# Performance work log

Measured on AMD Instinct MI355X. Metric: run time of the kernel, lower is better.

The kernel has to match this reference:

```python
import jax, jax.numpy as jnp
import numpy as np

B, L, LA, LL = 256, 512, 8, 64
V, D, P, HOPS = 100000, 300, 3, 3


def setup_inputs() -> dict:
    key = jax.random.key(0)
    ks = jax.random.split(key, 18)
    sc = 0.05
    return {
        "text":   jax.random.randint(ks[0], (B, L),  0, V),
        "aspect": jax.random.randint(ks[1], (B, LA), 0, V),
        "left":   jax.random.randint(ks[2], (B, LL), 0, V),
        # pretrained embedding table
        "embed": jax.random.normal(ks[3], (V, D), jnp.float32) * 0.1,
        # all Linear weights stored as [in, out] (y = x @ W + b)
        "Wx": jax.random.normal(ks[4], (D, D), jnp.float32) * sc,   # x_linear (no bias)
        "Ws": jax.random.normal(ks[5], (D, D), jnp.float32) * sc,   # s_linear (no bias)
        "Wk": jax.random.normal(ks[6], (D, D), jnp.float32) * sc,   # attention w_k
        "bk": jnp.zeros((D,), jnp.float32),
        "Wq": jax.random.normal(ks[7], (D, D), jnp.float32) * sc,   # attention w_q
        "bq": jnp.zeros((D,), jnp.float32),
        "w_mlp": jax.random.normal(ks[8], (2 * D,), jnp.float32) * sc,  # attention mlp score vector
        "Wproj": jax.random.normal(ks[9], (D, D), jnp.float32) * sc,    # attention proj
        "bproj": jnp.zeros((D,), jnp.float32),
        "Wm": jax.random.normal(ks[10], (D, D), jnp.float32) * sc,  # mlp
        "bm": jnp.zeros((D,), jnp.float32),
        "Wd": jax.random.normal(ks[11], (D, P), jnp.float32) * sc,  # dense
        "bd": jnp.zeros((P,), jnp.float32),
    }


def _forward(text, aspect, left, embed, Wx, Ws, Wk, bk, Wq, bq, w_mlp,
             Wproj, bproj, Wm, bm, Wd, bd):
    f32 = jnp.float32
    left_len = (left != 0).sum(-1)    # (B,)
    mem_len = (text != 0).sum(-1)     # (B,)
    asp_len = (aspect != 0).sum(-1)   # (B,)
    mem_len_f = mem_len.astype(f32)

    # aspect mean-pooled query (sum over all positions / nonzero count, as in torch code)
    asp_e = embed[aspect].sum(1) / asp_len.astype(f32)[:, None]   # (B, D)
    x = asp_e[:, None, :]                                         # (B, 1, D)

    memory = embed[text]                                          # (B, L, D)
    v_s = (memory.sum(1) / mem_len_f[:, None])[:, None, :]        # (B, 1, D)

    # SqueezeEmbedding (zero padding) + vectorized locationed_memory decay
    idx = jnp.arange(L, dtype=f32)[None, :]                       # (1, L)
    start = (left_len - asp_len).astype(f32)[:, None]             # aspect_start
    end = left_len.astype(f32)[:, None]                           # aspect_end
    l = jnp.where(idx < start, start - idx,
                  jnp.where(idx <= end, 0.0, idx - end))          # (B, L)
    w = 1.0 - l / mem_len_f[:, None]
    w = jnp.where(idx < mem_len_f[:, None], w, 0.0)               # zero padded positions
    memory = memory * w[:, :, None]                               # (B, L, D)

    for _ in range(HOPS):
        x = x @ Wx                                                # (B, 1, D)
        s = v_s @ Ws                                              # computed but unused (faithful)
        # Attention(score_function='mlp', n_head=1, hidden=D)
        kx = memory @ Wk + bk                                     # (B, L, D)
        qx = x @ Wq + bq                                          # (B, 1, D)
        # tanh(cat(kx, qx) @ w_mlp) == tanh(kx@w1 + qx@w2)
        score = jnp.tanh(kx @ w_mlp[:D] + qx @ w_mlp[D:])         # (B, L)
        score = jax.nn.softmax(score, axis=-1)
        v_ts = jnp.einsum('bl,bld->bd', score, kx)[:, None, :]    # (B, 1, D)
        v_ts = v_ts @ Wproj + bproj

    v_ns = (v_ts + v_s).reshape(text.shape[0], -1)                # (B, D)
    v_ms = jnp.tanh(v_ns @ Wm + bm)
    out = jax.nn.softmax(v_ms @ Wd + bd, axis=-1)                 # (B, P)
    return out


def reference(text, aspect, left, embed, Wx, Ws, Wk, bk, Wq, bq, w_mlp,
              Wproj, bproj, Wm, bm, Wd, bd):
    return _forward(text, aspect, left, embed, Wx, Ws, Wk, bk, Wq, bq,
                    w_mlp, Wproj, bproj, Wm, bm, Wd, bd)
```

## Files before the change

### kernel.cpp

```cpp
#include <hip/hip_runtime.h>
#include <math.h>

#define WS_KV 0
#define WS_C0 300
#define WS_C1 301
#define WS_H0 304
#define WS_H1 604
#define WS_MW 1024
#define WS_VS 77824

__device__ __forceinline__ float wred(float v) {
#pragma unroll
    for (int off = 32; off > 0; off >>= 1) v += __shfl_xor(v, off);
    return v;
}

__global__ __launch_bounds__(64) void k_prep(
    const float* __restrict__ Wk, const float* __restrict__ bk,
    const float* __restrict__ Wq, const float* __restrict__ bq,
    const float* __restrict__ wmlp, float* __restrict__ ws)
{
    const int lane = threadIdx.x;
    const int j = blockIdx.x;
    const float* u  = wmlp;
    const float* u2 = wmlp + 300;
    if (j < 300) {
        float pk = 0.f, pq = 0.f;
#pragma unroll
        for (int k = 0; k < 5; ++k) {
            int idx = lane + 64 * k;
            if (idx < 300) {
                pk += Wk[j * 300 + idx] * u[idx];
                pq += Wq[j * 300 + idx] * u2[idx];
            }
        }
        pk = wred(pk); pq = wred(pq);
        if (lane == 0) { ws[WS_KV + j] = pk; ws[WS_H0 + j] = pq; }
    } else if (j == 300) {
        float p = 0.f;
#pragma unroll
        for (int k = 0; k < 5; ++k) { int idx = lane + 64 * k; if (idx < 300) p += bk[idx] * u[idx]; }
        p = wred(p);
        if (lane == 0) ws[WS_C0] = p;
    } else {
        float p = 0.f;
#pragma unroll
        for (int k = 0; k < 5; ++k) { int idx = lane + 64 * k; if (idx < 300) p += bq[idx] * u2[idx]; }
        p = wred(p);
        if (lane == 0) ws[WS_C1] = p;
    }
}

__global__ __launch_bounds__(64) void k_hop(
    const float* __restrict__ Wx, const float* __restrict__ src,
    float* __restrict__ dst)
{
    const int lane = threadIdx.x;
    const int j = blockIdx.x;
    float p = 0.f;
#pragma unroll
    for (int k = 0; k < 5; ++k) {
        int idx = lane + 64 * k;
        if (idx < 300) p += Wx[j * 300 + idx] * src[idx];
    }
    p = wred(p);
    if (lane == 0) dst[j] = p;
}

__global__ __launch_bounds__(1024) void k_main(
    const int* __restrict__ text, const int* __restrict__ aspect,
    const int* __restrict__ left, const float* __restrict__ embed,
    float* __restrict__ ws)
{
    const int b = blockIdx.x;
    const int t = threadIdx.x;
    const int wv = t >> 6;
    const int lane = t & 63;

    __shared__ int   toks[512];
    __shared__ int   atoks[8];
    __shared__ float red[512];
    __shared__ __align__(16) float accW[16 * 300];
    __shared__ __align__(16) float vsW[16 * 300];
    __shared__ float denomW[16];
    __shared__ int   cnts[3];
    __shared__ float sc[4];

    if (t < 3) cnts[t] = 0;
    __syncthreads();

    bool predm = false, predl = false, preda = false;
    if (t < 512) { int tk = text[b * 512 + t]; toks[t] = tk; predm = (tk != 0); }
    else if (t < 576) predl = (left[b * 64 + (t - 512)] != 0);
    else if (t < 584) { int a = t - 576; int ak = aspect[b * 8 + a]; atoks[a] = ak; preda = (ak != 0); }
    {
        unsigned long long m;
        m = __ballot(predm); if (lane == 0 && m) atomicAdd(&cnts[0], __popcll(m));
        m = __ballot(predl); if (lane == 0 && m) atomicAdd(&cnts[1], __popcll(m));
        m = __ballot(preda); if (lane == 0 && m) atomicAdd(&cnts[2], __popcll(m));
    }
    __syncthreads();

    if (t < 300) {
        float s = 0.f;
#pragma unroll
        for (int a = 0; a < 8; ++a) s += embed[(size_t)atoks[a] * 300 + t];
        red[t] = (s / (float)cnts[2]) * ws[WS_H1 + t];
    } else if (t < 512) red[t] = 0.f;
    __syncthreads();
    for (int s = 256; s > 0; s >>= 1) { if (t < s) red[t] += red[t + s]; __syncthreads(); }
    if (t == 0) {
        sc[0] = (float)cnts[0];
        sc[1] = (float)(cnts[1] - cnts[2]);
        sc[2] = (float)cnts[1];
        sc[3] = red[0] + ws[WS_C0] + ws[WS_C1];
    }
    __syncthreads();
    const float mem_len_f = sc[0], startf = sc[1], endf = sc[2], qb = sc[3];

    const float4* kv4 = (const float4*)(ws + WS_KV);
    const float4* emb4 = (const float4*)embed;
    const bool hasB = (lane < 11);
    const float4 kva = kv4[lane];
    const float4 kvb = hasB ? kv4[64 + lane] : make_float4(0.f, 0.f, 0.f, 0.f);

    float4 accA = make_float4(0.f,0.f,0.f,0.f), accB = make_float4(0.f,0.f,0.f,0.f);
    float4 vsA  = make_float4(0.f,0.f,0.f,0.f), vsB  = make_float4(0.f,0.f,0.f,0.f);
    float denom = 0.f;

    for (int it = 0; it < 16; ++it) {
        const int l0 = wv * 32 + 2 * it, l1 = l0 + 1;
        const long r0 = (long)toks[l0] * 75, r1 = (long)toks[l1] * 75;
        float4 a0 = emb4[r0 + lane];
        float4 a1 = emb4[r1 + lane];
        float4 b0 = hasB ? emb4[r0 + 64 + lane] : make_float4(0.f,0.f,0.f,0.f);
        float4 b1 = hasB ? emb4[r1 + 64 + lane] : make_float4(0.f,0.f,0.f,0.f);

        float pd0 = a0.x*kva.x + a0.y*kva.y + a0.z*kva.z + a0.w*kva.w
                  + b0.x*kvb.x + b0.y*kvb.y + b0.z*kvb.z + b0.w*kvb.w;
        float pd1 = a1.x*kva.x + a1.y*kva.y + a1.z*kva.z + a1.w*kva.w
                  + b1.x*kvb.x + b1.y*kvb.y + b1.z*kvb.z + b1.w*kvb.w;
#pragma unroll
        for (int off = 32; off > 0; off >>= 1) {
            pd0 += __shfl_xor(pd0, off);
            pd1 += __shfl_xor(pd1, off);
        }

        const float f0 = (float)l0, f1 = (float)l1;
        float lv0 = (f0 < startf) ? (startf - f0) : ((f0 <= endf) ? 0.f : (f0 - endf));
        float lv1 = (f1 < startf) ? (startf - f1) : ((f1 <= endf) ? 0.f : (f1 - endf));
        float w0 = 1.f - lv0 / mem_len_f; w0 = (f0 < mem_len_f) ? w0 : 0.f;
        float w1 = 1.f - lv1 / mem_len_f; w1 = (f1 < mem_len_f) ? w1 : 0.f;

        const float p0 = expf(tanhf(w0 * pd0 + qb));
        const float p1 = expf(tanhf(w1 * pd1 + qb));
        const float pw0 = p0 * w0, pw1 = p1 * w1;

        accA.x += pw0*a0.x + pw1*a1.x;  accA.y += pw0*a0.y + pw1*a1.y;
        accA.z += pw0*a0.z + pw1*a1.z;  accA.w += pw0*a0.w + pw1*a1.w;
        accB.x += pw0*b0.x + pw1*b1.x;  accB.y += pw0*b0.y + pw1*b1.y;
        accB.z += pw0*b0.z + pw1*b1.z;  accB.w += pw0*b0.w + pw1*b1.w;
        vsA.x += a0.x + a1.x;  vsA.y += a0.y + a1.y;
        vsA.z += a0.z + a1.z;  vsA.w += a0.w + a1.w;
        vsB.x += b0.x + b1.x;  vsB.y += b0.y + b1.y;
        vsB.z += b0.z + b1.z;  vsB.w += b0.w + b1.w;
        denom += p0 + p1;
    }

    *(float4*)&accW[wv * 300 + 4 * lane] = accA;
    *(float4*)&vsW [wv * 300 + 4 * lane] = vsA;
    if (hasB) {
        *(float4*)&accW[wv * 300 + 256 + 4 * lane] = accB;
        *(float4*)&vsW [wv * 300 + 256 + 4 * lane] = vsB;
    }
    if (lane == 0) denomW[wv] = denom;
    __syncthreads();

    if (t < 300) {
        float ds = 0.f;
#pragma unroll
        for (int w = 0; w < 16; ++w) ds += denomW[w];
        float ms = 0.f, vs = 0.f;
#pragma unroll
        for (int w = 0; w < 16; ++w) { ms += accW[w * 300 + t]; vs += vsW[w * 300 + t]; }
        ws[WS_MW + b * 300 + t] = ms / ds;
        ws[WS_VS + b * 300 + t] = vs / mem_len_f;
    }
}

__global__ __launch_bounds__(960) void k_tail(
    const float* __restrict__ Wk, const float* __restrict__ bk,
    const float* __restrict__ Wproj, const float* __restrict__ bproj,
    const float* __restrict__ Wm, const float* __restrict__ bm,
    const float* __restrict__ Wd, const float* __restrict__ bd,
    float* __restrict__ out, const float* __restrict__ ws)
{
    const int t = threadIdx.x;
    const int b = blockIdx.x;
    const int seg = t / 320;
    const int j = t - seg * 320;

    __shared__ float A[300], T[300], part[900], vms[300], lg[3];

    if (t < 300) A[t] = ws[WS_MW + b * 300 + t];
    __syncthreads();

    if (j < 300) {
        const int k0 = seg * 100;
        float acc = 0.f;
#pragma unroll 10
        for (int i = 0; i < 100; ++i) acc += A[k0 + i] * Wk[(k0 + i) * 300 + j];
        part[seg * 300 + j] = acc;
    }
    __syncthreads();
    if (t < 300) T[t] = part[t] + part[300 + t] + part[600 + t] + bk[t];
    __syncthreads();

    if (j < 300) {
        const int k0 = seg * 100;
        float acc = 0.f;
#pragma unroll 10
        for (int i = 0; i < 100; ++i) acc += T[k0 + i] * Wproj[(k0 + i) * 300 + j];
        part[seg * 300 + j] = acc;
    }
    __syncthreads();
    if (t < 300) A[t] = part[t] + part[300 + t] + part[600 + t] + bproj[t] + ws[WS_VS + b * 300 + t];
    __syncthreads();

    if (j < 300) {
        const int k0 = seg * 100;
        float acc = 0.f;
#pragma unroll 10
        for (int i = 0; i < 100; ++i) acc += A[k0 + i] * Wm[(k0 + i) * 300 + j];
        part[seg * 300 + j] = acc;
    }
    __syncthreads();
    if (t < 300) vms[t] = tanhf(part[t] + part[300 + t] + part[600 + t] + bm[t]);
    __syncthreads();

    const int wv = t >> 6, lane = t & 63;
    if (wv < 3) {
        float p = 0.f;
#pragma unroll
        for (int k = 0; k < 5; ++k) { int d = lane + 64 * k; if (d < 300) p += vms[d] * Wd[d * 3 + wv]; }
        p = wred(p);
        if (lane == 0) lg[wv] = p + bd[wv];
    }
    __syncthreads();
    if (t == 0) {
        float l0 = lg[0], l1 = lg[1], l2 = lg[2];
        float mx = fmaxf(l0, fmaxf(l1, l2));
        float e0 = expf(l0 - mx), e1 = expf(l1 - mx), e2 = expf(l2 - mx);
        float s = e0 + e1 + e2;
        out[b * 3 + 0] = e0 / s;
        out[b * 3 + 1] = e1 / s;
        out[b * 3 + 2] = e2 / s;
    }
}

extern "C" void kernel_launch(void* const* d_in, const int* in_sizes, int n_in,
                              void* d_out, int out_size, void* d_ws, size_t ws_size,
                              hipStream_t stream)
{
    (void)in_sizes; (void)n_in; (void)out_size; (void)ws_size;
    const int*   text   = (const int*)d_in[0];
    const int*   aspect = (const int*)d_in[1];
    const int*   left   = (const int*)d_in[2];
    const float* embed  = (const float*)d_in[3];
    const float* Wx     = (const float*)d_in[4];
    const float* Wk     = (const float*)d_in[6];
    const float* bk     = (const float*)d_in[7];
    const float* Wq     = (const float*)d_in[8];
    const float* bq     = (const float*)d_in[9];
    const float* wmlp   = (const float*)d_in[10];
    const float* Wproj  = (const float*)d_in[11];
    const float* bproj  = (const float*)d_in[12];
    const float* Wm     = (const float*)d_in[13];
    const float* bm     = (const float*)d_in[14];
    const float* Wd     = (const float*)d_in[15];
    const float* bd     = (const float*)d_in[16];
    float* out = (float*)d_out;
    float* ws  = (float*)d_ws;

    hipLaunchKernelGGL(k_prep, dim3(302), dim3(64), 0, stream, Wk, bk, Wq, bq, wmlp, ws);
    hipLaunchKernelGGL(k_hop, dim3(300), dim3(64), 0, stream, Wx, ws + WS_H0, ws + WS_H1);
    hipLaunchKernelGGL(k_hop, dim3(300), dim3(64), 0, stream, Wx, ws + WS_H1, ws + WS_H0);
    hipLaunchKernelGGL(k_hop, dim3(300), dim3(64), 0, stream, Wx, ws + WS_H0, ws + WS_H1);
    hipLaunchKernelGGL(k_main, dim3(256), dim3(1024), 0, stream, text, aspect, left, embed, ws);
    hipLaunchKernelGGL(k_tail, dim3(256), dim3(960), 0, stream,
                       Wk, bk, Wproj, bproj, Wm, bm, Wd, bd, out, ws);
}
```

Baseline: 245.1 us.

## Split main gather across four blocks per batch and fuse prep/hop kernels

Merges the prep kernel and three hop kernels into a single one-block kernel that keeps hop vectors in shared memory, cutting four launches to one. The main kernel now uses 1024 blocks of 512 threads, each handling a quarter of the sequence, and writes unnormalised partial sums that the tail kernel combines and normalises. This raises parallelism across the GPU for the embedding gather and removes launch overhead. In exchange, the constant prep runs serially on one block, and the tail must read four times as many partial rows.

```diff
diff --git a/kernel.cpp b/kernel.cpp
--- a/kernel.cpp
+++ b/kernel.cpp
@@ -1,13 +1,13 @@
 #include <hip/hip_runtime.h>
 #include <math.h>
 
-#define WS_KV 0
-#define WS_C0 300
-#define WS_C1 301
-#define WS_H0 304
-#define WS_H1 604
-#define WS_MW 1024
-#define WS_VS 77824
+#define WS_KV   0
+#define WS_C0   300
+#define WS_C1   301
+#define WS_G    304
+#define WS_ACC  4096
+#define WS_VSP  311296
+#define WS_SCAL 618496
 
 __device__ __forceinline__ float wred(float v) {
 #pragma unroll
@@ -15,84 +15,94 @@
     return v;
 }
 
-__global__ __launch_bounds__(64) void k_prep(
-    const float* __restrict__ Wk, const float* __restrict__ bk,
-    const float* __restrict__ Wq, const float* __restrict__ bq,
-    const float* __restrict__ wmlp, float* __restrict__ ws)
+__global__ __launch_bounds__(1024) void k_const(
+    const float* __restrict__ Wx, const float* __restrict__ Wk,
+    const float* __restrict__ bk, const float* __restrict__ Wq,
+    const float* __restrict__ bq, const float* __restrict__ wmlp,
+    float* __restrict__ ws)
 {
-    const int lane = threadIdx.x;
-    const int j = blockIdx.x;
-    const float* u  = wmlp;
-    const float* u2 = wmlp + 300;
-    if (j < 300) {
+    const int t = threadIdx.x, wv = t >> 6, lane = t & 63;
+    __shared__ float uS[300], u2S[300], hA[300], hB[300];
+    if (t < 300) { uS[t] = wmlp[t]; u2S[t] = wmlp[300 + t]; }
+    __syncthreads();
+
+    for (int j = wv; j < 300; j += 16) {
         float pk = 0.f, pq = 0.f;
 #pragma unroll
-        for (int k = 0; k < 5; ++k) {
-            int idx = lane + 64 * k;
+        for (int m = 0; m < 5; ++m) {
+            int idx = lane + 64 * m;
             if (idx < 300) {
-                pk += Wk[j * 300 + idx] * u[idx];
-                pq += Wq[j * 300 + idx] * u2[idx];
+                pk += Wk[j * 300 + idx] * uS[idx];
+                pq += Wq[j * 300 + idx] * u2S[idx];
             }
         }
         pk = wred(pk); pq = wred(pq);
-        if (lane == 0) { ws[WS_KV + j] = pk; ws[WS_H0 + j] = pq; }
-    } else if (j == 300) {
+        if (lane == 0) { ws[WS_KV + j] = pk; hA[j] = pq; }
+    }
+    if (wv == 0) {
         float p = 0.f;
 #pragma unroll
-        for (int k = 0; k < 5; ++k) { int idx = lane + 64 * k; if (idx < 300) p += bk[idx] * u[idx]; }
+        for (int m = 0; m < 5; ++m) { int idx = lane + 64 * m; if (idx < 300) p += bk[idx] * uS[idx]; }
         p = wred(p);
         if (lane == 0) ws[WS_C0] = p;
-    } else {
+    }
+    if (wv == 1) {
         float p = 0.f;
 #pragma unroll
-        for (int k = 0; k < 5; ++k) { int idx = lane + 64 * k; if (idx < 300) p += bq[idx] * u2[idx]; }
+        for (int m = 0; m < 5; ++m) { int idx = lane + 64 * m; if (idx < 300) p += bq[idx] * u2S[idx]; }
         p = wred(p);
         if (lane == 0) ws[WS_C1] = p;
     }
-}
-
-__global__ __launch_bounds__(64) void k_hop(
-    const float* __restrict__ Wx, const float* __restrict__ src,
-    float* __restrict__ dst)
-{
-    const int lane = threadIdx.x;
-    const int j = blockIdx.x;
-    float p = 0.f;
-#pragma unroll
-    for (int k = 0; k < 5; ++k) {
-        int idx = lane + 64 * k;
-        if (idx < 300) p += Wx[j * 300 + idx] * src[idx];
-    }
-    p = wred(p);
-    if (lane == 0) dst[j] = p;
-}
-
-__global__ __launch_bounds__(1024) void k_main(
+    __syncthreads();
+
+#pragma unroll
+    for (int hop = 0; hop < 3; ++hop) {
+        const float* src = (hop & 1) ? hB : hA;
+        float* dst = (hop & 1) ? hA : hB;
+        for (int j = wv; j < 300; j += 16) {
+            float p = 0.f;
+#pragma unroll
+            for (int m = 0; m < 5; ++m) {
+                int idx = lane + 64 * m;
+                if (idx < 300) p += Wx[j * 300 + idx] * src[idx];
+            }
+            p = wred(p);
+            if (lane == 0) dst[j] = p;
+        }
+        __syncthreads();
+    }
+    if (t < 300) ws[WS_G + t] = hB[t];
+}
+
+__global__ __launch_bounds__(512, 6) void k_main(
     const int* __restrict__ text, const int* __restrict__ aspect,
     const int* __restrict__ left, const float* __restrict__ embed,
     float* __restrict__ ws)
 {
-    const int b = blockIdx.x;
-    const int t = threadIdx.x;
-    const int wv = t >> 6;
-    const int lane = t & 63;
-
-    __shared__ int   toks[512];
-    __shared__ int   atoks[8];
-    __shared__ float red[512];
-    __shared__ __align__(16) float accW[16 * 300];
-    __shared__ __align__(16) float vsW[16 * 300];
-    __shared__ float denomW[16];
+    const int bid = blockIdx.x;
+    const int b = bid >> 2, quarter = bid & 3;
+    const int t = threadIdx.x, wv = t >> 6, lane = t & 63;
+
+    __shared__ int   toksS[128];
+    __shared__ int   atoksS[8];
+    __shared__ __align__(16) float accW[8 * 300];
+    __shared__ __align__(16) float vsW[8 * 300];
+    __shared__ float denomW[8], qpart[5], sc[4];
     __shared__ int   cnts[3];
-    __shared__ float sc[4];
 
     if (t < 3) cnts[t] = 0;
     __syncthreads();
 
-    bool predm = false, predl = false, preda = false;
-    if (t < 512) { int tk = text[b * 512 + t]; toks[t] = tk; predm = (tk != 0); }
-    else if (t < 576) predl = (left[b * 64 + (t - 512)] != 0);
-    else if (t < 584) { int a = t - 576; int ak = aspect[b * 8 + a]; atoks[a] = ak; preda = (ak != 0); }
+    const int tk = text[b * 512 + t];
+    const bool predm = (tk != 0);
+    if ((t >> 7) == quarter) toksS[t & 127] = tk;
+    const bool predl = (t < 64) && (left[b * 64 + t] != 0);
+    bool preda = false;
+    if (t >= 64 && t < 72) {
+        int ak = aspect[b * 8 + (t - 64)];
+        atoksS[t - 64] = ak;
+        preda = (ak != 0);
+    }
     {
         unsigned long long m;
         m = __ballot(predm); if (lane == 0 && m) atomicAdd(&cnts[0], __popcll(m));
@@ -101,24 +111,29 @@
     }
     __syncthreads();
 
-    if (t < 300) {
-        float s = 0.f;
-#pragma unroll
-        for (int a = 0; a < 8; ++a) s += embed[(size_t)atoks[a] * 300 + t];
-        red[t] = (s / (float)cnts[2]) * ws[WS_H1 + t];
-    } else if (t < 512) red[t] = 0.f;
-    __syncthreads();
-    for (int s = 256; s > 0; s >>= 1) { if (t < s) red[t] += red[t + s]; __syncthreads(); }
+    if (wv < 5) {
+        float val = 0.f;
+        if (t < 300) {
+            float s = 0.f;
+#pragma unroll
+            for (int a = 0; a < 8; ++a) s += embed[(size_t)atoksS[a] * 300 + t];
+            val = s * ws[WS_G + t];
+        }
+        val = wred(val);
+        if (lane == 0) qpart[wv] = val;
+    }
+    __syncthreads();
     if (t == 0) {
+        float q = (qpart[0] + qpart[1] + qpart[2] + qpart[3] + qpart[4]) / (float)cnts[2];
         sc[0] = (float)cnts[0];
         sc[1] = (float)(cnts[1] - cnts[2]);
         sc[2] = (float)cnts[1];
-        sc[3] = red[0] + ws[WS_C0] + ws[WS_C1];
+        sc[3] = q + ws[WS_C0] + ws[WS_C1];
     }
     __syncthreads();
     const float mem_len_f = sc[0], startf = sc[1], endf = sc[2], qb = sc[3];
 
-    const float4* kv4 = (const float4*)(ws + WS_KV);
+    const float4* kv4  = (const float4*)(ws + WS_KV);
     const float4* emb4 = (const float4*)embed;
     const bool hasB = (lane < 11);
     const float4 kva = kv4[lane];
@@ -127,10 +142,11 @@
     float4 accA = make_float4(0.f,0.f,0.f,0.f), accB = make_float4(0.f,0.f,0.f,0.f);
     float4 vsA  = make_float4(0.f,0.f,0.f,0.f), vsB  = make_float4(0.f,0.f,0.f,0.f);
     float denom = 0.f;
-
-    for (int it = 0; it < 16; ++it) {
-        const int l0 = wv * 32 + 2 * it, l1 = l0 + 1;
-        const long r0 = (long)toks[l0] * 75, r1 = (long)toks[l1] * 75;
+    const float posbase = (float)(quarter * 128);
+
+    for (int it = 0; it < 8; ++it) {
+        const int l0 = wv * 16 + 2 * it, l1 = l0 + 1;
+        const int r0 = toksS[l0] * 75, r1 = toksS[l1] * 75;
         float4 a0 = emb4[r0 + lane];
         float4 a1 = emb4[r1 + lane];
         float4 b0 = hasB ? emb4[r0 + 64 + lane] : make_float4(0.f,0.f,0.f,0.f);
@@ -146,7 +162,7 @@
             pd1 += __shfl_xor(pd1, off);
         }
 
-        const float f0 = (float)l0, f1 = (float)l1;
+        const float f0 = posbase + (float)l0, f1 = f0 + 1.f;
         float lv0 = (f0 < startf) ? (startf - f0) : ((f0 <= endf) ? 0.f : (f0 - endf));
         float lv1 = (f1 < startf) ? (startf - f1) : ((f1 <= endf) ? 0.f : (f1 - endf));
         float w0 = 1.f - lv0 / mem_len_f; w0 = (f0 < mem_len_f) ? w0 : 0.f;
@@ -179,12 +195,13 @@
     if (t < 300) {
         float ds = 0.f;
 #pragma unroll
-        for (int w = 0; w < 16; ++w) ds += denomW[w];
+        for (int w = 0; w < 8; ++w) ds += denomW[w];
         float ms = 0.f, vs = 0.f;
 #pragma unroll
-        for (int w = 0; w < 16; ++w) { ms += accW[w * 300 + t]; vs += vsW[w * 300 + t]; }
-        ws[WS_MW + b * 300 + t] = ms / ds;
-        ws[WS_VS + b * 300 + t] = vs / mem_len_f;
+        for (int w = 0; w < 8; ++w) { ms += accW[w * 300 + t]; vs += vsW[w * 300 + t]; }
+        ws[WS_ACC + bid * 300 + t] = ms;
+        ws[WS_VSP + bid * 300 + t] = vs;
+        if (t == 0) { ws[WS_SCAL + bid * 2] = ds; ws[WS_SCAL + bid * 2 + 1] = mem_len_f; }
     }
 }
 
@@ -197,12 +214,23 @@
 {
     const int t = threadIdx.x;
     const int b = blockIdx.x;
-    const int seg = t / 320;
-    const int j = t - seg * 320;
-
-    __shared__ float A[300], T[300], part[900], vms[300], lg[3];
-
-    if (t < 300) A[t] = ws[WS_MW + b * 300 + t];
+    const int seg = t / 320, j = t - seg * 320;
+
+    __shared__ float A[300], T[300], VSs[300], part[900], vms[300], lg[3];
+
+    if (t < 300) {
+        const int p0 = (b * 4) * 300 + t;
+        float a = ws[WS_ACC + p0] + ws[WS_ACC + p0 + 300]
+                + ws[WS_ACC + p0 + 600] + ws[WS_ACC + p0 + 900];
+        float v = ws[WS_VSP + p0] + ws[WS_VSP + p0 + 300]
+                + ws[WS_VSP + p0 + 600] + ws[WS_VSP + p0 + 900];
+        const int s0 = b * 8;
+        float d  = ws[WS_SCAL + s0] + ws[WS_SCAL + s0 + 2]
+                 + ws[WS_SCAL + s0 + 4] + ws[WS_SCAL + s0 + 6];
+        float ml = ws[WS_SCAL + s0 + 1];
+        A[t]   = a / d;
+        VSs[t] = v / ml;
+    }
     __syncthreads();
 
     if (j < 300) {
@@ -224,7 +252,7 @@
         part[seg * 300 + j] = acc;
     }
     __syncthreads();
-    if (t < 300) A[t] = part[t] + part[300 + t] + part[600 + t] + bproj[t] + ws[WS_VS + b * 300 + t];
+    if (t < 300) A[t] = part[t] + part[300 + t] + part[600 + t] + bproj[t] + VSs[t];
     __syncthreads();
 
     if (j < 300) {
@@ -282,11 +310,10 @@
     float* out = (float*)d_out;
     float* ws  = (float*)d_ws;
 
-    hipLaunchKernelGGL(k_prep, dim3(302), dim3(64), 0, stream, Wk, bk, Wq, bq, wmlp, ws);
-    hipLaunchKernelGGL(k_hop, dim3(300), dim3(64), 0, stream, Wx, ws + WS_H0, ws + WS_H1);
-    hipLaunchKernelGGL(k_hop, dim3(300), dim3(64), 0, stream, Wx, ws + WS_H1, ws + WS_H0);
-    hipLaunchKernelGGL(k_hop, dim3(300), dim3(64), 0, stream, Wx, ws + WS_H0, ws + WS_H1);
-    hipLaunchKernelGGL(k_main, dim3(256), dim3(1024), 0, stream, text, aspect, left, embed, ws);
+    hipLaunchKernelGGL(k_const, dim3(1), dim3(1024), 0, stream,
+                       Wx, Wk, bk, Wq, bq, wmlp, ws);
+    hipLaunchKernelGGL(k_main, dim3(1024), dim3(512), 0, stream,
+                       text, aspect, left, embed, ws);
     hipLaunchKernelGGL(k_tail, dim3(256), dim3(960), 0, stream,
                        Wk, bk, Wproj, bproj, Wm, bm, Wd, bd, out, ws);
 }
```

Result: slower. 303.2 us (+23.7%).
